# Kernel tuning notes

Hardware: AMD Instinct MI355X
Metric: run time of the kernel (lower is better)

Reference implementation:

```python
import jax, jax.numpy as jnp
import numpy as np

B, T, D, H = 4, 4096, 1024, 16
HD = D // H  # head_dim = 64


def setup_inputs() -> dict:
    key = jax.random.key(0)
    k1, k2, k3 = jax.random.split(key, 3)
    x = jax.random.normal(k1, (B, T, D), dtype=jnp.float32)
    # torch Linear weight is (out,in); we store transposed (in,out) for x @ W
    Wqkv = jax.random.normal(k2, (D, 3 * D), dtype=jnp.float32) * 0.02
    Wout = jax.random.normal(k3, (D, D), dtype=jnp.float32) * 0.02
    return {"x": x, "Wqkv": Wqkv, "Wout": Wout}


def reference(x, Wqkv, Wout):
    # Faithful to original: qkv reshaped to (B,T,3,H,hd) WITHOUT moving heads to
    # a batch dim, so attention mixes the H heads of each token (scores: B,T,H,H).
    qkv = (x @ Wqkv).reshape(B, T, 3, H, HD)
    q, k, v = qkv[:, :, 0], qkv[:, :, 1], qkv[:, :, 2]  # each (B,T,H,HD)
    scores = jnp.einsum('btid,btjd->btij', q, k) / jnp.sqrt(jnp.float32(HD))
    attn = jax.nn.softmax(scores, axis=-1)  # softmax over heads j
    out = jnp.einsum('btij,btjd->btid', attn, v).reshape(B, T, D)
    return out @ Wout
```

## Files before the change

kernel.cpp:

```cpp
#include <hip/hip_runtime.h>
#include <hip/hip_bf16.h>
#include <cstdint>
#include <cstddef>


typedef __bf16 bf16x8 __attribute__((ext_vector_type(8)));
typedef __bf16 bf16x4 __attribute__((ext_vector_type(4)));
typedef float  f32x4  __attribute__((ext_vector_type(4)));

#define AS1 __attribute__((address_space(1)))
#define AS3 __attribute__((address_space(3)))

__device__ __forceinline__ void async_copy16(const void* g, void* l) {
    __builtin_amdgcn_global_load_lds((const AS1 void*)g, (AS3 void*)l, 16, 0, 0);
}

__device__ __forceinline__ int invp_qkv(int col) {
    int g = col >> 10;
    if (g == 2) { int q = col & 1023; return 2048 + ((q & 63) << 4) + (q >> 6); }
    int h = (col >> 6) & 15, d = col & 63;
    return (g << 10) + ((d & 32) << 4) + (((d >> 3) & 3) << 7) + (h << 3) + (d & 7);
}

__device__ __forceinline__ int invp_ao(int k) {
    return (((k >> 8) & 3) << 8) + ((k & 15) << 4) + (((k >> 4) & 3) << 2) + ((k >> 6) & 3);
}

__global__ __launch_bounds__(256) void cvt_bf16_kernel(const float4* __restrict__ in,
                                                       bf16x4* __restrict__ out, int n4) {
    int i = blockIdx.x * 256 + threadIdx.x;
    if (i >= n4) return;
    float4 v = in[i];
    bf16x4 o = { (__bf16)v.x, (__bf16)v.y, (__bf16)v.z, (__bf16)v.w };
    out[i] = o;
}

__global__ __launch_bounds__(256) void transpose_qkv_kernel(const float* __restrict__ in,
                                                            __bf16* __restrict__ out) {
    __shared__ float tile[32][33];
    const int C = 3072;
    int c0 = blockIdx.x * 32, r0 = blockIdx.y * 32;
    int tx = threadIdx.x, ty = threadIdx.y;
    #pragma unroll
    for (int i = 0; i < 32; i += 8)
        tile[ty + i][tx] = in[(size_t)(r0 + ty + i) * C + c0 + tx];
    __syncthreads();
    #pragma unroll
    for (int i = 0; i < 32; i += 8) {
        int prow = invp_qkv(c0 + ty + i);
        out[(size_t)prow * 1024 + r0 + tx] = (__bf16)tile[tx][ty + i];
    }
}

__global__ __launch_bounds__(256) void transpose_wout_kernel(const float* __restrict__ in,
                                                             __bf16* __restrict__ out) {
    __shared__ float tile[32][33];
    const int C = 1024;
    int c0 = blockIdx.x * 32, r0 = blockIdx.y * 32;
    int tx = threadIdx.x, ty = threadIdx.y;
    #pragma unroll
    for (int i = 0; i < 32; i += 8)
        tile[ty + i][tx] = in[(size_t)(r0 + ty + i) * C + c0 + tx];
    __syncthreads();
    int pk = invp_ao(r0 + tx);
    #pragma unroll
    for (int i = 0; i < 32; i += 8)
        out[(size_t)(c0 + ty + i) * 1024 + pk] = (__bf16)tile[tx][ty + i];
}

template<int OUT_BF16>
__global__ __launch_bounds__(512) void gemm_bt(const __bf16* __restrict__ A,
                                               const __bf16* __restrict__ Bt,
                                               void* __restrict__ Cv,
                                               int N, int K) {
    __shared__ __attribute__((aligned(16))) __bf16 As[4 * 256 * 32];
    __shared__ __attribute__((aligned(16))) __bf16 Bs[4 * 256 * 32];

    const int lin = blockIdx.x;
    const int xcd = lin & 7;
    const int rr  = lin >> 3;
    const int by  = xcd * 8 + (rr & 7);
    const int bx  = rr >> 3;

    const int tid  = threadIdx.x;
    const int wave = tid >> 6;
    const int lane = tid & 63;
    const int quad = lane >> 4;
    const int q16  = lane & 15;
    const int wr   = wave >> 2, wc = wave & 3;
    const int row0 = by * 256;
    const int col0 = bx * 256;

    const __bf16* Ag = A  + (size_t)row0 * K;
    const __bf16* Bg = Bt + (size_t)col0 * K;

    const int srow = tid >> 2;
    const int sk   = ((tid & 3) ^ ((srow >> 1) & 3)) << 3;
    const __bf16* aSrc = Ag + (size_t)srow * K + sk;
    const __bf16* bSrc = Bg + (size_t)srow * K + sk;
    char* aDst = (char*)As + tid * 16;
    char* bDst = (char*)Bs + tid * 16;

    const int pxo  = (quad ^ ((q16 >> 1) & 3)) << 4;
    const int aoff = wr * 8192 + q16 * 64 + pxo;
    const int boff = wc * 4096 + q16 * 64 + pxo;

    f32x4 acc[8][4] = {};

    const int NT = K >> 5;

#define STAGE(t, g) do { \
        const size_t so = (size_t)(g) * 128 * K + (size_t)(t) * 32; \
        const int   dof = ((t) & 3) * 16384 + (g) * 8192; \
        async_copy16(aSrc + so, aDst + dof); \
        async_copy16(bSrc + so, bDst + dof); \
    } while (0)

    STAGE(0, 0); STAGE(0, 1);
    STAGE(1, 0); STAGE(1, 1);
    STAGE(2, 0); STAGE(2, 1);
    asm volatile("s_waitcnt vmcnt(8)" ::: "memory");
    __builtin_amdgcn_s_barrier();
    __builtin_amdgcn_sched_barrier(0);

    #pragma unroll 1
    for (int t = 0; t < NT; ++t) {
        const char* Ab = (const char*)As + (t & 3) * 16384;
        const char* Bb = (const char*)Bs + (t & 3) * 16384;
        const bool pf = (t + 3 < NT);

        bf16x8 bf[4], af[4];
        #pragma unroll
        for (int ni = 0; ni < 4; ++ni)
            bf[ni] = *(const bf16x8*)(Bb + boff + ni * 1024);
        #pragma unroll
        for (int mi = 0; mi < 4; ++mi)
            af[mi] = *(const bf16x8*)(Ab + aoff + mi * 1024);
        if (pf) STAGE(t + 3, 0);
        __builtin_amdgcn_sched_barrier(0);
        __builtin_amdgcn_s_barrier();
        asm volatile("s_waitcnt lgkmcnt(0)" ::: "memory");
        __builtin_amdgcn_sched_barrier(0);
        __builtin_amdgcn_s_setprio(1);
        #pragma unroll
        for (int mi = 0; mi < 4; ++mi)
            #pragma unroll
            for (int ni = 0; ni < 4; ++ni)
                acc[mi][ni] = __builtin_amdgcn_mfma_f32_16x16x32_bf16(af[mi], bf[ni], acc[mi][ni], 0, 0, 0);
        __builtin_amdgcn_s_setprio(0);
        __builtin_amdgcn_sched_barrier(0);
        __builtin_amdgcn_s_barrier();

        bf16x8 a2[4];
        #pragma unroll
        for (int mi = 0; mi < 4; ++mi)
            a2[mi] = *(const bf16x8*)(Ab + 4096 + aoff + mi * 1024);
        if (pf) STAGE(t + 3, 1);
        __builtin_amdgcn_sched_barrier(0);
        __builtin_amdgcn_s_barrier();
        asm volatile("s_waitcnt lgkmcnt(0)" ::: "memory");
        __builtin_amdgcn_sched_barrier(0);
        __builtin_amdgcn_s_setprio(1);
        #pragma unroll
        for (int mi = 0; mi < 4; ++mi)
            #pragma unroll
            for (int ni = 0; ni < 4; ++ni)
                acc[mi + 4][ni] = __builtin_amdgcn_mfma_f32_16x16x32_bf16(a2[mi], bf[ni], acc[mi + 4][ni], 0, 0, 0);
        __builtin_amdgcn_s_setprio(0);
        __builtin_amdgcn_sched_barrier(0);
        if (t < NT - 3)       asm volatile("s_waitcnt vmcnt(8)" ::: "memory");
        else if (t == NT - 3) asm volatile("s_waitcnt vmcnt(4)" ::: "memory");
        else                  asm volatile("s_waitcnt vmcnt(0)" ::: "memory");
        __builtin_amdgcn_s_barrier();
        __builtin_amdgcn_sched_barrier(0);
    }
#undef STAGE

    #pragma unroll
    for (int mi = 0; mi < 8; ++mi) {
        #pragma unroll
        for (int ni = 0; ni < 4; ++ni) {
            const int col = col0 + wc * 64 + ni * 16 + q16;
            #pragma unroll
            for (int r = 0; r < 4; ++r) {
                const int row = row0 + wr * 128 + mi * 16 + quad * 4 + r;
                if (OUT_BF16)
                    ((__bf16*)Cv)[(size_t)row * N + col] = (__bf16)acc[mi][ni][r];
                else
                    ((float*)Cv)[(size_t)row * N + col] = acc[mi][ni][r];
            }
        }
    }
}

__global__ __launch_bounds__(256) void attn_mfma_kernel(const __bf16* __restrict__ qkv,
                                                        __bf16* __restrict__ ao) {
    const int tok  = blockIdx.x * 4 + (threadIdx.x >> 6);
    const int lane = threadIdx.x & 63;
    const int quad = lane >> 4;
    const int q16  = lane & 15;

    const __bf16* base = qkv + (size_t)tok * 3072;

    const bf16x8 qf0 = *(const bf16x8*)(base + lane * 8);
    const bf16x8 qf1 = *(const bf16x8*)(base + 512 + lane * 8);
    const bf16x8 kf0 = *(const bf16x8*)(base + 1024 + lane * 8);
    const bf16x8 kf1 = *(const bf16x8*)(base + 1536 + lane * 8);

    f32x4 st = {0.f, 0.f, 0.f, 0.f};
    st = __builtin_amdgcn_mfma_f32_16x16x32_bf16(kf0, qf0, st, 0, 0, 0);
    st = __builtin_amdgcn_mfma_f32_16x16x32_bf16(kf1, qf1, st, 0, 0, 0);

    float s0 = st[0] * 0.125f, s1 = st[1] * 0.125f, s2 = st[2] * 0.125f, s3 = st[3] * 0.125f;
    float m = fmaxf(fmaxf(s0, s1), fmaxf(s2, s3));
    m = fmaxf(m, __shfl_xor(m, 16));
    m = fmaxf(m, __shfl_xor(m, 32));
    float e0 = __expf(s0 - m), e1 = __expf(s1 - m), e2 = __expf(s2 - m), e3 = __expf(s3 - m);
    float sum = e0 + e1 + e2 + e3;
    sum += __shfl_xor(sum, 16);
    sum += __shfl_xor(sum, 32);
    const float inv = 1.f / sum;

    union { __bf16 h[2]; int i; } u01, u23;
    u01.h[0] = (__bf16)(e0 * inv); u01.h[1] = (__bf16)(e1 * inv);
    u23.h[0] = (__bf16)(e2 * inv); u23.h[1] = (__bf16)(e3 * inv);

    const int src0 = quad * 32 + q16;
    const int src1 = src0 + 16;
    union { int i[4]; bf16x8 v; } af;
    af.i[0] = __shfl(u01.i, src0);
    af.i[1] = __shfl(u23.i, src0);
    af.i[2] = __shfl(u01.i, src1);
    af.i[3] = __shfl(u23.i, src1);
    if (quad >= 2) { af.i[0] = 0; af.i[1] = 0; af.i[2] = 0; af.i[3] = 0; }

    const __bf16* vb = base + 2048;
    f32x4 accs[4];
    #pragma unroll
    for (int c = 0; c < 4; ++c) {
        bf16x8 bfv = {};
        if (quad < 2)
            bfv = *(const bf16x8*)(vb + (c * 16 + q16) * 16 + quad * 8);
        f32x4 z = {0.f, 0.f, 0.f, 0.f};
        accs[c] = __builtin_amdgcn_mfma_f32_16x16x32_bf16(af.v, bfv, z, 0, 0, 0);
    }

    union { __bf16 h[16]; bf16x8 v[2]; } o;
    #pragma unroll
    for (int c = 0; c < 4; ++c)
        #pragma unroll
        for (int r = 0; r < 4; ++r)
            o.h[c * 4 + r] = (__bf16)accs[c][r];
    __bf16* outp = ao + (size_t)tok * 1024 + lane * 16;
    *(bf16x8*)outp = o.v[0];
    *(bf16x8*)(outp + 8) = o.v[1];
}

extern "C" void kernel_launch(void* const* d_in, const int* in_sizes, int n_in,
                              void* d_out, int out_size, void* d_ws, size_t ws_size,
                              hipStream_t stream) {
    const float* x    = (const float*)d_in[0];
    const float* Wqkv = (const float*)d_in[1];
    const float* Wout = (const float*)d_in[2];
    float* out = (float*)d_out;

    char* ws = (char*)d_ws;
    __bf16* xb    = (__bf16*)(ws);
    __bf16* wqkvT = (__bf16*)(ws + 33554432);
    __bf16* woutT = (__bf16*)(ws + 33554432 + 6291456);
    __bf16* qkv   = (__bf16*)(ws + 33554432 + 6291456 + 2097152);
    __bf16* ao    = (__bf16*)(ws + 33554432 + 6291456 + 2097152 + 100663296);

    cvt_bf16_kernel<<<16384, 256, 0, stream>>>((const float4*)x, (bf16x4*)xb, 4194304);
    transpose_qkv_kernel<<<dim3(96, 32), dim3(32, 8), 0, stream>>>(Wqkv, wqkvT);
    transpose_wout_kernel<<<dim3(32, 32), dim3(32, 8), 0, stream>>>(Wout, woutT);
    gemm_bt<1><<<768, 512, 0, stream>>>(xb, wqkvT, (void*)qkv, 3072, 1024);
    attn_mfma_kernel<<<4096, 256, 0, stream>>>(qkv, ao);
    gemm_bt<0><<<256, 512, 0, stream>>>(ao, woutT, (void*)out, 1024, 1024);
}
```

Measured before the change: 308.5 us.

## Software-pipeline LDS fragment loads with MFMA using ping-pong register buffers

Restructures the GEMM main loop so the LDS fragment reads for the next K tile are issued while the current tile's MFMAs run. Two register sets alternate between even and odd iterations, the loop is unrolled by two, and the vmcnt wait points are moved. It also adds a launch bound of two blocks per CU. The aim is to hide LDS latency and cut barrier stalls, at the cost of more registers, which could force spills under the tighter occupancy bound. The loop also assumes NT is even.

```diff
diff --git a/kernel.cpp b/kernel.cpp
--- a/kernel.cpp
+++ b/kernel.cpp
@@ -69,10 +69,10 @@
 }
 
 template<int OUT_BF16>
-__global__ __launch_bounds__(512) void gemm_bt(const __bf16* __restrict__ A,
-                                               const __bf16* __restrict__ Bt,
-                                               void* __restrict__ Cv,
-                                               int N, int K) {
+__global__ __launch_bounds__(512, 2) void gemm_bt(const __bf16* __restrict__ A,
+                                                  const __bf16* __restrict__ Bt,
+                                                  void* __restrict__ Cv,
+                                                  int N, int K) {
     __shared__ __attribute__((aligned(16))) __bf16 As[4 * 256 * 32];
     __shared__ __attribute__((aligned(16))) __bf16 Bs[4 * 256 * 32];
 
@@ -110,10 +110,10 @@
     const int NT = K >> 5;
 
 #define STAGE(t, g) do { \
-        const size_t so = (size_t)(g) * 128 * K + (size_t)(t) * 32; \
-        const int   dof = ((t) & 3) * 16384 + (g) * 8192; \
-        async_copy16(aSrc + so, aDst + dof); \
-        async_copy16(bSrc + so, bDst + dof); \
+        const size_t so_ = (size_t)(g) * 128 * K + (size_t)(t) * 32; \
+        const int   dof_ = ((t) & 3) * 16384 + (g) * 8192; \
+        async_copy16(aSrc + so_, aDst + dof_); \
+        async_copy16(bSrc + so_, bDst + dof_); \
     } while (0)
 
     STAGE(0, 0); STAGE(0, 1);
@@ -123,57 +123,74 @@
     __builtin_amdgcn_s_barrier();
     __builtin_amdgcn_sched_barrier(0);
 
+    bf16x8 bfA[4], bfB[4], a03A[4], a03B[4], a47[4];
+    #pragma unroll
+    for (int ni = 0; ni < 4; ++ni)
+        bfA[ni] = *(const bf16x8*)((const char*)Bs + boff + ni * 1024);
+    #pragma unroll
+    for (int mi = 0; mi < 4; ++mi)
+        a03A[mi] = *(const bf16x8*)((const char*)As + aoff + mi * 1024);
+    asm volatile("s_waitcnt lgkmcnt(0)" ::: "memory");
+    __builtin_amdgcn_sched_barrier(0);
+
+#define TILE_STEP(T, BFC, A03C, BFN, A03N) do { \
+        const int t_ = (T); \
+        const char* Ab_ = (const char*)As + (t_ & 3) * 16384; \
+        const char* Bb_ = (const char*)Bs + (t_ & 3) * 16384; \
+         \
+        _Pragma("unroll") \
+        for (int mi = 0; mi < 4; ++mi) \
+            a47[mi] = *(const bf16x8*)(Ab_ + 4096 + aoff + mi * 1024); \
+        if (t_ + 3 < NT) STAGE(t_ + 3, 0); \
+        __builtin_amdgcn_sched_barrier(0); \
+        if (t_ < NT - 3)       asm volatile("s_waitcnt vmcnt(6)" ::: "memory"); \
+        else if (t_ == NT - 3) asm volatile("s_waitcnt vmcnt(4)" ::: "memory"); \
+        else                   asm volatile("s_waitcnt vmcnt(0)" ::: "memory"); \
+        __builtin_amdgcn_s_barrier(); \
+        __builtin_amdgcn_sched_barrier(0); \
+        __builtin_amdgcn_s_setprio(1); \
+        _Pragma("unroll") \
+        for (int mi = 0; mi < 4; ++mi) \
+            _Pragma("unroll") \
+            for (int ni = 0; ni < 4; ++ni) \
+                acc[mi][ni] = __builtin_amdgcn_mfma_f32_16x16x32_bf16(A03C[mi], BFC[ni], acc[mi][ni], 0, 0, 0); \
+        __builtin_amdgcn_s_setprio(0); \
+        __builtin_amdgcn_sched_barrier(0); \
+        asm volatile("s_waitcnt lgkmcnt(0)" ::: "memory"); \
+        __builtin_amdgcn_sched_barrier(0); \
+         \
+        if (t_ + 1 < NT) { \
+            const char* Ab1_ = (const char*)As + ((t_ + 1) & 3) * 16384; \
+            const char* Bb1_ = (const char*)Bs + ((t_ + 1) & 3) * 16384; \
+            _Pragma("unroll") \
+            for (int ni = 0; ni < 4; ++ni) \
+                BFN[ni] = *(const bf16x8*)(Bb1_ + boff + ni * 1024); \
+            _Pragma("unroll") \
+            for (int mi = 0; mi < 4; ++mi) \
+                A03N[mi] = *(const bf16x8*)(Ab1_ + aoff + mi * 1024); \
+        } \
+        if (t_ + 3 < NT) STAGE(t_ + 3, 1); \
+        __builtin_amdgcn_sched_barrier(0); \
+        __builtin_amdgcn_s_barrier(); \
+        __builtin_amdgcn_sched_barrier(0); \
+        __builtin_amdgcn_s_setprio(1); \
+        _Pragma("unroll") \
+        for (int mi = 0; mi < 4; ++mi) \
+            _Pragma("unroll") \
+            for (int ni = 0; ni < 4; ++ni) \
+                acc[mi + 4][ni] = __builtin_amdgcn_mfma_f32_16x16x32_bf16(a47[mi], BFC[ni], acc[mi + 4][ni], 0, 0, 0); \
+        __builtin_amdgcn_s_setprio(0); \
+        __builtin_amdgcn_sched_barrier(0); \
+        asm volatile("s_waitcnt lgkmcnt(0)" ::: "memory"); \
+        __builtin_amdgcn_sched_barrier(0); \
+    } while (0)
+
     #pragma unroll 1
-    for (int t = 0; t < NT; ++t) {
-        const char* Ab = (const char*)As + (t & 3) * 16384;
-        const char* Bb = (const char*)Bs + (t & 3) * 16384;
-        const bool pf = (t + 3 < NT);
-
-        bf16x8 bf[4], af[4];
-        #pragma unroll
-        for (int ni = 0; ni < 4; ++ni)
-            bf[ni] = *(const bf16x8*)(Bb + boff + ni * 1024);
-        #pragma unroll
-        for (int mi = 0; mi < 4; ++mi)
-            af[mi] = *(const bf16x8*)(Ab + aoff + mi * 1024);
-        if (pf) STAGE(t + 3, 0);
-        __builtin_amdgcn_sched_barrier(0);
-        __builtin_amdgcn_s_barrier();
-        asm volatile("s_waitcnt lgkmcnt(0)" ::: "memory");
-        __builtin_amdgcn_sched_barrier(0);
-        __builtin_amdgcn_s_setprio(1);
-        #pragma unroll
-        for (int mi = 0; mi < 4; ++mi)
-            #pragma unroll
-            for (int ni = 0; ni < 4; ++ni)
-                acc[mi][ni] = __builtin_amdgcn_mfma_f32_16x16x32_bf16(af[mi], bf[ni], acc[mi][ni], 0, 0, 0);
-        __builtin_amdgcn_s_setprio(0);
-        __builtin_amdgcn_sched_barrier(0);
-        __builtin_amdgcn_s_barrier();
-
-        bf16x8 a2[4];
-        #pragma unroll
-        for (int mi = 0; mi < 4; ++mi)
-            a2[mi] = *(const bf16x8*)(Ab + 4096 + aoff + mi * 1024);
-        if (pf) STAGE(t + 3, 1);
-        __builtin_amdgcn_sched_barrier(0);
-        __builtin_amdgcn_s_barrier();
-        asm volatile("s_waitcnt lgkmcnt(0)" ::: "memory");
-        __builtin_amdgcn_sched_barrier(0);
-        __builtin_amdgcn_s_setprio(1);
-        #pragma unroll
-        for (int mi = 0; mi < 4; ++mi)
-            #pragma unroll
-            for (int ni = 0; ni < 4; ++ni)
-                acc[mi + 4][ni] = __builtin_amdgcn_mfma_f32_16x16x32_bf16(a2[mi], bf[ni], acc[mi + 4][ni], 0, 0, 0);
-        __builtin_amdgcn_s_setprio(0);
-        __builtin_amdgcn_sched_barrier(0);
-        if (t < NT - 3)       asm volatile("s_waitcnt vmcnt(8)" ::: "memory");
-        else if (t == NT - 3) asm volatile("s_waitcnt vmcnt(4)" ::: "memory");
-        else                  asm volatile("s_waitcnt vmcnt(0)" ::: "memory");
-        __builtin_amdgcn_s_barrier();
-        __builtin_amdgcn_sched_barrier(0);
-    }
+    for (int t = 0; t < NT; t += 2) {
+        TILE_STEP(t,     bfA, a03A, bfB, a03B);
+        TILE_STEP(t + 1, bfB, a03B, bfA, a03A);
+    }
+#undef TILE_STEP
 #undef STAGE
 
     #pragma unroll
```

Measured after the change: 302.7 us. No clear change (-1.9%).

## Shrink GEMM tile to 256x128 with triple-buffered single-barrier pipeline

Applied to the files above, without the earlier changes.

Reduces the GEMM block tile from 256x256 to 256x128, with 8 waves arranged 4x2. Each wave now computes a 64x64 output, so the accumulator shrinks to half its former size. The LDS pipeline goes from four buffers with split A half-stages and several barriers per step to three buffers with one barrier per k-step, and setprio is removed. Grid sizes double so more blocks fit per CU, and launch_bounds asks for 4 waves per SIMD. This trades lower per-block arithmetic intensity and more global reads of A for higher occupancy and a simpler schedule.

```diff
diff --git a/kernel.cpp b/kernel.cpp
--- a/kernel.cpp
+++ b/kernel.cpp
@@ -69,12 +69,12 @@
 }
 
 template<int OUT_BF16>
-__global__ __launch_bounds__(512) void gemm_bt(const __bf16* __restrict__ A,
-                                               const __bf16* __restrict__ Bt,
-                                               void* __restrict__ Cv,
-                                               int N, int K) {
-    __shared__ __attribute__((aligned(16))) __bf16 As[4 * 256 * 32];
-    __shared__ __attribute__((aligned(16))) __bf16 Bs[4 * 256 * 32];
+__global__ __launch_bounds__(512, 4) void gemm_bt(const __bf16* __restrict__ A,
+                                                  const __bf16* __restrict__ Bt,
+                                                  void* __restrict__ Cv,
+                                                  int N, int K) {
+    __shared__ __attribute__((aligned(16))) __bf16 As[3 * 256 * 32];
+    __shared__ __attribute__((aligned(16))) __bf16 Bs[3 * 128 * 32];
 
     const int lin = blockIdx.x;
     const int xcd = lin & 7;
@@ -87,9 +87,9 @@
     const int lane = tid & 63;
     const int quad = lane >> 4;
     const int q16  = lane & 15;
-    const int wr   = wave >> 2, wc = wave & 3;
+    const int wr   = wave >> 1, wc = wave & 1;
     const int row0 = by * 256;
-    const int col0 = bx * 256;
+    const int col0 = bx * 128;
 
     const __bf16* Ag = A  + (size_t)row0 * K;
     const __bf16* Bg = Bt + (size_t)col0 * K;
@@ -102,88 +102,61 @@
     char* bDst = (char*)Bs + tid * 16;
 
     const int pxo  = (quad ^ ((q16 >> 1) & 3)) << 4;
-    const int aoff = wr * 8192 + q16 * 64 + pxo;
+    const int aoff = wr * 4096 + q16 * 64 + pxo;
     const int boff = wc * 4096 + q16 * 64 + pxo;
 
-    f32x4 acc[8][4] = {};
+    f32x4 acc[4][4] = {};
 
     const int NT = K >> 5;
 
-#define STAGE(t, g) do { \
-        const size_t so = (size_t)(g) * 128 * K + (size_t)(t) * 32; \
-        const int   dof = ((t) & 3) * 16384 + (g) * 8192; \
-        async_copy16(aSrc + so, aDst + dof); \
-        async_copy16(bSrc + so, bDst + dof); \
+#define STAGE(t) do { \
+        const size_t so_ = (size_t)(t) * 32; \
+        const int   sl_  = (t) % 3; \
+        async_copy16(aSrc + so_,                 aDst + sl_ * 16384); \
+        async_copy16(aSrc + (size_t)128 * K + so_, aDst + sl_ * 16384 + 8192); \
+        async_copy16(bSrc + so_,                 bDst + sl_ * 8192); \
     } while (0)
 
-    STAGE(0, 0); STAGE(0, 1);
-    STAGE(1, 0); STAGE(1, 1);
-    STAGE(2, 0); STAGE(2, 1);
-    asm volatile("s_waitcnt vmcnt(8)" ::: "memory");
+    STAGE(0);
+    STAGE(1);
+    asm volatile("s_waitcnt vmcnt(3)" ::: "memory");
     __builtin_amdgcn_s_barrier();
     __builtin_amdgcn_sched_barrier(0);
 
     #pragma unroll 1
     for (int t = 0; t < NT; ++t) {
-        const char* Ab = (const char*)As + (t & 3) * 16384;
-        const char* Bb = (const char*)Bs + (t & 3) * 16384;
-        const bool pf = (t + 3 < NT);
-
-        bf16x8 bf[4], af[4];
+        if (t + 2 < NT) STAGE(t + 2);
+        const int slot = t % 3;
+        const char* Ab = (const char*)As + slot * 16384;
+        const char* Bb = (const char*)Bs + slot * 8192;
+        bf16x8 af[4], bf[4];
+        #pragma unroll
+        for (int mi = 0; mi < 4; ++mi)
+            af[mi] = *(const bf16x8*)(Ab + aoff + mi * 1024);
         #pragma unroll
         for (int ni = 0; ni < 4; ++ni)
             bf[ni] = *(const bf16x8*)(Bb + boff + ni * 1024);
-        #pragma unroll
-        for (int mi = 0; mi < 4; ++mi)
-            af[mi] = *(const bf16x8*)(Ab + aoff + mi * 1024);
-        if (pf) STAGE(t + 3, 0);
-        __builtin_amdgcn_sched_barrier(0);
-        __builtin_amdgcn_s_barrier();
-        asm volatile("s_waitcnt lgkmcnt(0)" ::: "memory");
-        __builtin_amdgcn_sched_barrier(0);
-        __builtin_amdgcn_s_setprio(1);
         #pragma unroll
         for (int mi = 0; mi < 4; ++mi)
             #pragma unroll
             for (int ni = 0; ni < 4; ++ni)
                 acc[mi][ni] = __builtin_amdgcn_mfma_f32_16x16x32_bf16(af[mi], bf[ni], acc[mi][ni], 0, 0, 0);
-        __builtin_amdgcn_s_setprio(0);
         __builtin_amdgcn_sched_barrier(0);
-        __builtin_amdgcn_s_barrier();
-
-        bf16x8 a2[4];
-        #pragma unroll
-        for (int mi = 0; mi < 4; ++mi)
-            a2[mi] = *(const bf16x8*)(Ab + 4096 + aoff + mi * 1024);
-        if (pf) STAGE(t + 3, 1);
-        __builtin_amdgcn_sched_barrier(0);
-        __builtin_amdgcn_s_barrier();
-        asm volatile("s_waitcnt lgkmcnt(0)" ::: "memory");
-        __builtin_amdgcn_sched_barrier(0);
-        __builtin_amdgcn_s_setprio(1);
-        #pragma unroll
-        for (int mi = 0; mi < 4; ++mi)
-            #pragma unroll
-            for (int ni = 0; ni < 4; ++ni)
-                acc[mi + 4][ni] = __builtin_amdgcn_mfma_f32_16x16x32_bf16(a2[mi], bf[ni], acc[mi + 4][ni], 0, 0, 0);
-        __builtin_amdgcn_s_setprio(0);
-        __builtin_amdgcn_sched_barrier(0);
-        if (t < NT - 3)       asm volatile("s_waitcnt vmcnt(8)" ::: "memory");
-        else if (t == NT - 3) asm volatile("s_waitcnt vmcnt(4)" ::: "memory");
-        else                  asm volatile("s_waitcnt vmcnt(0)" ::: "memory");
+        if (t < NT - 2) asm volatile("s_waitcnt vmcnt(3)" ::: "memory");
+        else            asm volatile("s_waitcnt vmcnt(0)" ::: "memory");
         __builtin_amdgcn_s_barrier();
         __builtin_amdgcn_sched_barrier(0);
     }
 #undef STAGE
 
     #pragma unroll
-    for (int mi = 0; mi < 8; ++mi) {
+    for (int mi = 0; mi < 4; ++mi) {
         #pragma unroll
         for (int ni = 0; ni < 4; ++ni) {
             const int col = col0 + wc * 64 + ni * 16 + q16;
             #pragma unroll
             for (int r = 0; r < 4; ++r) {
-                const int row = row0 + wr * 128 + mi * 16 + quad * 4 + r;
+                const int row = row0 + wr * 64 + mi * 16 + quad * 4 + r;
                 if (OUT_BF16)
                     ((__bf16*)Cv)[(size_t)row * N + col] = (__bf16)acc[mi][ni][r];
                 else
@@ -274,7 +247,7 @@
     cvt_bf16_kernel<<<16384, 256, 0, stream>>>((const float4*)x, (bf16x4*)xb, 4194304);
     transpose_qkv_kernel<<<dim3(96, 32), dim3(32, 8), 0, stream>>>(Wqkv, wqkvT);
     transpose_wout_kernel<<<dim3(32, 32), dim3(32, 8), 0, stream>>>(Wout, woutT);
-    gemm_bt<1><<<768, 512, 0, stream>>>(xb, wqkvT, (void*)qkv, 3072, 1024);
+    gemm_bt<1><<<1536, 512, 0, stream>>>(xb, wqkvT, (void*)qkv, 3072, 1024);
     attn_mfma_kernel<<<4096, 256, 0, stream>>>(qkv, ao);
-    gemm_bt<0><<<256, 512, 0, stream>>>(ao, woutT, (void*)out, 1024, 1024);
-}
+    gemm_bt<0><<<512, 512, 0, stream>>>(ao, woutT, (void*)out, 1024, 1024);
+}
```

Result: slower. 314.7 us (+2.0%).
